# Kernel optimization log

Hardware: AMD Instinct MI355X
Metric: run time of the kernel (lower is better)

The kernel has to match this reference:

```python
import jax, jax.numpy as jnp
import numpy as np

N, D, H, F = 4096, 512, 8, 2048
DH = D // H
EPS = 1e-5


def layer_norm(x, g, b):
    mu = jnp.mean(x, axis=-1, keepdims=True)
    var = jnp.var(x, axis=-1, keepdims=True)
    return (x - mu) * jax.lax.rsqrt(var + EPS) * g + b


def setup_inputs() -> dict:
    key = jax.random.key(0)
    ks = jax.random.split(key, 16)
    s = 0.02
    return {
        "x": jax.random.normal(ks[0], (N, D), jnp.float32),
        "attention_bias": jax.random.normal(ks[1], (N, N, H), jnp.float32),
        "ln1_g": jnp.ones((D,), jnp.float32),
        "ln1_b": jnp.zeros((D,), jnp.float32),
        "wq": jax.random.normal(ks[2], (D, D), jnp.float32) * s,
        "bq": jnp.zeros((D,), jnp.float32),
        "wk": jax.random.normal(ks[3], (D, D), jnp.float32) * s,
        "bk": jnp.zeros((D,), jnp.float32),
        "wv": jax.random.normal(ks[4], (D, D), jnp.float32) * s,
        "bv": jnp.zeros((D,), jnp.float32),
        "wo": jax.random.normal(ks[5], (D, D), jnp.float32) * s,
        "bo": jnp.zeros((D,), jnp.float32),
        "ln2_g": jnp.ones((D,), jnp.float32),
        "ln2_b": jnp.zeros((D,), jnp.float32),
        "w1": jax.random.normal(ks[6], (D, F), jnp.float32) * s,
        "b1": jnp.zeros((F,), jnp.float32),
        "w2": jax.random.normal(ks[7], (F, D), jnp.float32) * s,
        "b2": jnp.zeros((D,), jnp.float32),
    }


def reference(x, attention_bias, ln1_g, ln1_b, wq, bq, wk, bk, wv, bv, wo, bo,
              ln2_g, ln2_b, w1, b1, w2, b2):
    # --- Pre-LN attention block ---
    residual = x
    xn = layer_norm(x, ln1_g, ln1_b)
    q = (xn @ wq + bq).reshape(N, H, DH)
    k = (xn @ wk + bk).reshape(N, H, DH)
    v = (xn @ wv + bv).reshape(N, H, DH)
    # scores: (H, N, N)
    scores = jnp.einsum("nhd,mhd->hnm", q, k) / jnp.sqrt(jnp.float32(DH))
    scores = scores + jnp.transpose(attention_bias, (2, 0, 1))
    attn = jax.nn.softmax(scores, axis=-1)
    ctx = jnp.einsum("hnm,mhd->nhd", attn, v).reshape(N, D)
    x = residual + (ctx @ wo + bo)
    # --- Pre-LN FFN block ---
    residual = x
    xn = layer_norm(x, ln2_g, ln2_b)
    h = jax.nn.gelu(xn @ w1 + b1, approximate=False)
    x = residual + (h @ w2 + b2)
    return x
```

## Files before the change

kernel.cpp:

```cpp
#include <hip/hip_runtime.h>


typedef float f32x4 __attribute__((ext_vector_type(4)));
typedef short s8v  __attribute__((ext_vector_type(8)));
typedef unsigned short u16;

#define MFMA16(a,b,c) __builtin_amdgcn_mfma_f32_16x16x32_bf16((a),(b),(c),0,0,0)

static constexpr int N  = 4096;
static constexpr int D  = 512;
static constexpr int H  = 8;
static constexpr int F  = 2048;
static constexpr int QKVW = 3 * D;
static constexpr int NH   = N * H;
static constexpr int QT   = 64;
static constexpr int MS   = 4;
static constexpr int ATTN_LDS = 131072;

__device__ inline u16 f2bf(float f) {
  union { float f; unsigned u; } x; x.f = f;
  unsigned r = x.u + 0x7fffu + ((x.u >> 16) & 1u);
  return (u16)(r >> 16);
}
__device__ inline float bf2f(u16 u) {
  union { unsigned u; float f; } x; x.u = ((unsigned)u) << 16;
  return x.f;
}

typedef const unsigned __attribute__((address_space(1)))* gp_t;
typedef unsigned __attribute__((address_space(3)))* lp_t;
__device__ inline void gl_lds16(const void* g, void* l) {
  __builtin_amdgcn_global_load_lds((gp_t)g, (lp_t)l, 16, 0, 0);
}

__global__ __launch_bounds__(256) void ln_kernel(const float* __restrict__ x,
                                                 const float* __restrict__ g,
                                                 const float* __restrict__ b,
                                                 u16* __restrict__ out) {
  const int row  = blockIdx.x * 4 + (threadIdx.x >> 6);
  const int lane = threadIdx.x & 63;
  const float4* xr = (const float4*)(x + (size_t)row * D);
  float4 v0 = xr[lane], v1 = xr[64 + lane];
  float s  = v0.x + v0.y + v0.z + v0.w + v1.x + v1.y + v1.z + v1.w;
  float ss = v0.x*v0.x + v0.y*v0.y + v0.z*v0.z + v0.w*v0.w
           + v1.x*v1.x + v1.y*v1.y + v1.z*v1.z + v1.w*v1.w;
  for (int off = 1; off < 64; off <<= 1) {
    s  += __shfl_xor(s,  off);
    ss += __shfl_xor(ss, off);
  }
  const float mu   = s * (1.0f / D);
  const float var  = ss * (1.0f / D) - mu * mu;
  const float rstd = rsqrtf(var + 1e-5f);
  const float4* g4 = (const float4*)g;
  const float4* b4 = (const float4*)b;
  float4 g0 = g4[lane], g1 = g4[64 + lane];
  float4 b0 = b4[lane], b1 = b4[64 + lane];
  u16* orow = out + (size_t)row * D;
  ushort4 o0, o1;
  o0.x = f2bf((v0.x - mu) * rstd * g0.x + b0.x);
  o0.y = f2bf((v0.y - mu) * rstd * g0.y + b0.y);
  o0.z = f2bf((v0.z - mu) * rstd * g0.z + b0.z);
  o0.w = f2bf((v0.w - mu) * rstd * g0.w + b0.w);
  o1.x = f2bf((v1.x - mu) * rstd * g1.x + b1.x);
  o1.y = f2bf((v1.y - mu) * rstd * g1.y + b1.y);
  o1.z = f2bf((v1.z - mu) * rstd * g1.z + b1.z);
  o1.w = f2bf((v1.w - mu) * rstd * g1.w + b1.w);
  ((ushort4*)orow)[lane]      = o0;
  ((ushort4*)orow)[64 + lane] = o1;
}

__global__ __launch_bounds__(256) void transpose_all(
    const float* __restrict__ wq, const float* __restrict__ wk,
    const float* __restrict__ wv, const float* __restrict__ wo,
    const float* __restrict__ w1, const float* __restrict__ w2,
    u16* __restrict__ WqkvT, u16* __restrict__ WoT,
    u16* __restrict__ W1T, u16* __restrict__ W2T) {
  __shared__ u16 tl[32][33];
  const int b = blockIdx.x;
  const float* src; u16* dst; int R, C, tb;
  if (b < 768)       { int m = b >> 8; tb = b & 255;
                       src = (m == 0) ? wq : (m == 1) ? wk : wv;
                       dst = WqkvT + m * D * D; R = D; C = D; }
  else if (b < 1024) { tb = b - 768;  src = wo; dst = WoT; R = D; C = D; }
  else if (b < 2048) { tb = b - 1024; src = w1; dst = W1T; R = D; C = F; }
  else               { tb = b - 2048; src = w2; dst = W2T; R = F; C = D; }
  const int tx = C / 32;
  const int cb = tb % tx, rb = tb / tx;
  const int c = threadIdx.x & 31, r8 = threadIdx.x >> 5;
#pragma unroll
  for (int i = 0; i < 4; i++) {
    int r = r8 + i * 8;
    tl[r][c] = f2bf(src[(size_t)(rb * 32 + r) * C + cb * 32 + c]);
  }
  __syncthreads();
#pragma unroll
  for (int i = 0; i < 4; i++) {
    int r = r8 + i * 8;
    dst[(size_t)(cb * 32 + r) * R + rb * 32 + c] = tl[c][r];
  }
}

__global__ void pack_bqkv(const float* __restrict__ bq, const float* __restrict__ bk,
                          const float* __restrict__ bv, float* __restrict__ bqkv) {
  int i = blockIdx.x * 256 + threadIdx.x;
  if (i < QKVW) bqkv[i] = (i < D) ? bq[i] : (i < 2 * D) ? bk[i - D] : bv[i - 2 * D];
}

__global__ void make_kvtiles(const u16* __restrict__ qkv,
                             u16* __restrict__ kt, u16* __restrict__ vt) {
  if (blockIdx.x < 1024) {
    int t = blockIdx.x * 256 + threadIdx.x;
    int ln = t & 63, half = (t >> 6) & 1, h = (t >> 7) & 7, mt = t >> 10;
    int lr = ln & 15, lq = ln >> 4;
    const u16* src = qkv + (size_t)(mt * 16 + lr) * QKVW + D + h * 64 + half * 32 + lq * 8;
    *(int4*)(kt + (size_t)t * 8) = *(const int4*)src;
  } else {
    int t = (blockIdx.x - 1024) * 256 + threadIdx.x;
    int ln = t & 63, db = (t >> 6) & 3, h = (t >> 8) & 7, mt32 = t >> 11;
    int lr = ln & 15, lq = ln >> 4;
    s8v v;
#pragma unroll
    for (int e = 0; e < 8; e++) {
      int msrc = 4 * lq + 16 * (e >> 2) + (e & 3);
      v[e] = (short)qkv[(size_t)(mt32 * 32 + msrc) * QKVW + 2 * D + h * 64 + db * 16 + lr];
    }
    *(s8v*)(vt + (size_t)t * 8) = v;
  }
}

template <int MODE>
__global__ __launch_bounds__(256) void gemm_bt(const u16* __restrict__ A,
                                               const u16* __restrict__ Bt,
                                               const float* __restrict__ bias,
                                               const float* __restrict__ res,
                                               void* __restrict__ outv,
                                               int M, int Nn, int K) {
  __shared__ __align__(16) u16 As[128 * 32];
  __shared__ __align__(16) u16 Bs[128 * 32];
  const int t = threadIdx.x;
  const int lane = t & 63, w = t >> 6;
  const int wr = w >> 1, wc = w & 1;
  const int lr = lane & 15, lq = lane >> 4;
  const int r0 = blockIdx.y * 128, c0 = blockIdx.x * 128;
  const int srow = lane >> 2, scc = (lane & 3) * 8;
  f32x4 acc[4][4] = {};
  for (int k0 = 0; k0 < K; k0 += 32) {
    __syncthreads();
#pragma unroll
    for (int s = w; s < 8; s += 4) {
      gl_lds16(&A[(size_t)(r0 + s * 16 + srow) * K + k0 + scc], &As[s * 512]);
      gl_lds16(&Bt[(size_t)(c0 + s * 16 + srow) * K + k0 + scc], &Bs[s * 512]);
    }
    __syncthreads();
    s8v af[4], bf[4];
#pragma unroll
    for (int m = 0; m < 4; m++) af[m] = *(const s8v*)&As[(wr * 64 + m * 16 + lr) * 32 + lq * 8];
#pragma unroll
    for (int n = 0; n < 4; n++) bf[n] = *(const s8v*)&Bs[(wc * 64 + n * 16 + lr) * 32 + lq * 8];
#pragma unroll
    for (int m = 0; m < 4; m++)
#pragma unroll
      for (int n = 0; n < 4; n++) acc[m][n] = MFMA16(af[m], bf[n], acc[m][n]);
  }
#pragma unroll
  for (int m = 0; m < 4; m++)
#pragma unroll
    for (int n = 0; n < 4; n++) {
      const int col = c0 + wc * 64 + n * 16 + lr;
      const float bcol = bias[col];
#pragma unroll
      for (int j = 0; j < 4; j++) {
        const int row = r0 + wr * 64 + m * 16 + lq * 4 + j;
        float v = acc[m][n][j] + bcol;
        if (MODE == 0) {
          ((u16*)outv)[(size_t)row * Nn + col] = f2bf(v);
        } else if (MODE == 1) {
          v = 0.5f * v * (1.0f + erff(v * 0.70710678118654752f));
          ((u16*)outv)[(size_t)row * Nn + col] = f2bf(v);
        } else {
          ((float*)outv)[(size_t)row * Nn + col] = v + res[(size_t)row * Nn + col];
        }
      }
    }
  (void)M;
}

__global__ __launch_bounds__(256) void gemm_bt64(const u16* __restrict__ A,
                                                 const u16* __restrict__ Bt,
                                                 const float* __restrict__ bias,
                                                 const float* __restrict__ res,
                                                 float* __restrict__ out,
                                                 int M, int Nn, int K) {
  __shared__ __align__(16) u16 As[64 * 32];
  __shared__ __align__(16) u16 Bs[128 * 32];
  const int t = threadIdx.x;
  const int lane = t & 63, w = t >> 6;
  const int wr = w >> 1, wc = w & 1;
  const int lr = lane & 15, lq = lane >> 4;
  const int r0 = blockIdx.y * 64, c0 = blockIdx.x * 128;
  const int srow = lane >> 2, scc = (lane & 3) * 8;
  f32x4 acc[2][4] = {};
  for (int k0 = 0; k0 < K; k0 += 32) {
    __syncthreads();
    gl_lds16(&A[(size_t)(r0 + w * 16 + srow) * K + k0 + scc], &As[w * 512]);
#pragma unroll
    for (int s = w; s < 8; s += 4)
      gl_lds16(&Bt[(size_t)(c0 + s * 16 + srow) * K + k0 + scc], &Bs[s * 512]);
    __syncthreads();
    s8v af[2], bf[4];
#pragma unroll
    for (int m = 0; m < 2; m++) af[m] = *(const s8v*)&As[(wr * 32 + m * 16 + lr) * 32 + lq * 8];
#pragma unroll
    for (int n = 0; n < 4; n++) bf[n] = *(const s8v*)&Bs[(wc * 64 + n * 16 + lr) * 32 + lq * 8];
#pragma unroll
    for (int m = 0; m < 2; m++)
#pragma unroll
      for (int n = 0; n < 4; n++) acc[m][n] = MFMA16(af[m], bf[n], acc[m][n]);
  }
#pragma unroll
  for (int m = 0; m < 2; m++)
#pragma unroll
    for (int n = 0; n < 4; n++) {
      const int col = c0 + wc * 64 + n * 16 + lr;
      const float bcol = bias[col];
#pragma unroll
      for (int j = 0; j < 4; j++) {
        const int row = r0 + wr * 32 + m * 16 + lq * 4 + j;
        out[(size_t)row * Nn + col] = acc[m][n][j] + bcol + res[(size_t)row * Nn + col];
      }
    }
  (void)M;
}

__global__ __launch_bounds__(512, 2) void attn_kernel(const u16* __restrict__ qkv,
                                                      const u16* __restrict__ kt,
                                                      const u16* __restrict__ vt,
                                                      const float* __restrict__ bias,
                                                      u16* __restrict__ ctxp,
                                                      float* __restrict__ ml) {
  extern __shared__ __align__(16) char smem[];
  const int tid = threadIdx.x, lane = tid & 63, h = tid >> 6;
  const int lr = lane & 15, lq = lane >> 4;
  const int bid = blockIdx.x;
  const int ms = (bid & 7) >> 1;
  const int qb = ((bid >> 3) << 1) | (bid & 1);
  const int q0 = qb * QT;
  const int mt32_0 = ms * 32;

  float4 breg[8];
  auto load_bias = [&](int t) {
#pragma unroll
    for (int i = 0; i < 8; i++) {
      int g = i * 512 + tid;
      int q = g >> 6, cc = g & 63;
      breg[i] = *(const float4*)(bias + (size_t)(q0 + q) * NH
                + (size_t)((mt32_0 + t) * 32 + (cc >> 1)) * H + (cc & 1) * 4);
    }
  };
  auto write_bias = [&](int buf) {
    float* bl = (float*)(smem + buf * 65536);
#pragma unroll
    for (int i = 0; i < 8; i++) {
      int g = i * 512 + tid;
      int q = g >> 6, cc = g & 63;
      int m = cc >> 1, h0 = (cc & 1) * 4;
      int mp = m ^ ((q & 7) << 2);
#pragma unroll
      for (int e = 0; e < 4; e++)
        bl[q * 256 + (h0 + e) * 32 + mp] = breg[i][e];
    }
  };

  s8v qf[4][2];
#pragma unroll
  for (int qc = 0; qc < 4; qc++) {
    const u16* qp = qkv + (size_t)(q0 + qc * 16 + lr) * QKVW + h * 64 + lq * 8;
    qf[qc][0] = *(const s8v*)qp;
    qf[qc][1] = *(const s8v*)(qp + 32);
  }

  f32x4 cacc[4][4] = {};
  float mrun[4], lsum[4];
#pragma unroll
  for (int qc = 0; qc < 4; qc++) { mrun[qc] = -1e30f; lsum[qc] = 0.0f; }

  load_bias(0);
  write_bias(0);
  __syncthreads();

  for (int t = 0; t < 32; t++) {
    const int mt = (mt32_0 + t) * 2;
    s8v kf[4];
    {
      const u16* kp0 = kt + ((size_t)(mt * 8 + h) * 2) * 512 + lane * 8;
      const u16* kp1 = kt + ((size_t)((mt + 1) * 8 + h) * 2) * 512 + lane * 8;
      kf[0] = *(const s8v*)kp0;
      kf[1] = *(const s8v*)(kp0 + 512);
      kf[2] = *(const s8v*)kp1;
      kf[3] = *(const s8v*)(kp1 + 512);
    }
    s8v vf[4];
    {
      const u16* vp = vt + ((size_t)((mt32_0 + t) * 8 + h) * 4) * 512 + lane * 8;
#pragma unroll
      for (int db = 0; db < 4; db++) vf[db] = *(const s8v*)(vp + (size_t)db * 512);
    }
    if (t + 1 < 32) load_bias(t + 1);

    const float* bl = (const float*)(smem + (t & 1) * 65536);
#pragma unroll
    for (int qc = 0; qc < 4; qc++) {
      f32x4 s0 = {}, s1 = {};
      s0 = MFMA16(kf[0], qf[qc][0], s0);
      s0 = MFMA16(kf[1], qf[qc][1], s0);
      s1 = MFMA16(kf[2], qf[qc][0], s1);
      s1 = MFMA16(kf[3], qf[qc][1], s1);
      const int q = qc * 16 + lr;
      const int sw = (q & 7) << 2;
      const float* blq = bl + q * 256 + h * 32;
      float p[8];
      float tmax = -1e30f;
#pragma unroll
      for (int s = 0; s < 2; s++) {
        f32x4 b4 = *(const f32x4*)(blq + ((s * 16 + lq * 4) ^ sw));
#pragma unroll
        for (int j = 0; j < 4; j++) {
          const float sv = (s ? s1[j] : s0[j]) * 0.125f + b4[j];
          p[s * 4 + j] = sv;
          tmax = fmaxf(tmax, sv);
        }
      }
      tmax = fmaxf(tmax, __shfl_xor(tmax, 16));
      tmax = fmaxf(tmax, __shfl_xor(tmax, 32));
      if (!__all(tmax <= mrun[qc])) {
        float mnew = fmaxf(mrun[qc], tmax);
        float sc = __expf(mrun[qc] - mnew);
        mrun[qc] = mnew;
        lsum[qc] *= sc;
#pragma unroll
        for (int db = 0; db < 4; db++) cacc[qc][db] *= sc;
      }
      float psum = 0.0f;
#pragma unroll
      for (int j = 0; j < 8; j++) { p[j] = __expf(p[j] - mrun[qc]); psum += p[j]; }
      lsum[qc] += psum;
      union { unsigned u[4]; s8v v; } pa;
      asm("v_cvt_pk_bf16_f32 %0, %1, %2" : "=v"(pa.u[0]) : "v"(p[0]), "v"(p[1]));
      asm("v_cvt_pk_bf16_f32 %0, %1, %2" : "=v"(pa.u[1]) : "v"(p[2]), "v"(p[3]));
      asm("v_cvt_pk_bf16_f32 %0, %1, %2" : "=v"(pa.u[2]) : "v"(p[4]), "v"(p[5]));
      asm("v_cvt_pk_bf16_f32 %0, %1, %2" : "=v"(pa.u[3]) : "v"(p[6]), "v"(p[7]));
#pragma unroll
      for (int db = 0; db < 4; db++) cacc[qc][db] = MFMA16(vf[db], pa.v, cacc[qc][db]);
    }
    if (t + 1 < 32) write_bias((t + 1) & 1);
    __syncthreads();
  }

#pragma unroll
  for (int qc = 0; qc < 4; qc++) {
    lsum[qc] += __shfl_xor(lsum[qc], 16);
    lsum[qc] += __shfl_xor(lsum[qc], 32);
  }
  if (lq == 0) {
#pragma unroll
    for (int qc = 0; qc < 4; qc++) {
      float2 v = make_float2(mrun[qc], lsum[qc]);
      *(float2*)(ml + (((size_t)ms * N + q0 + qc * 16 + lr) * H + h) * 2) = v;
    }
  }
#pragma unroll
  for (int qc = 0; qc < 4; qc++)
#pragma unroll
    for (int db = 0; db < 4; db++) {
      const size_t q = q0 + qc * 16 + lr;
      ushort4 r4;
      r4.x = f2bf(cacc[qc][db][0]);
      r4.y = f2bf(cacc[qc][db][1]);
      r4.z = f2bf(cacc[qc][db][2]);
      r4.w = f2bf(cacc[qc][db][3]);
      *(ushort4*)(ctxp + ((size_t)ms * N + q) * D + h * 64 + db * 16 + lq * 4) = r4;
    }
}

__global__ __launch_bounds__(256) void attn_merge(const u16* __restrict__ ctxp,
                                                  const float* __restrict__ ml,
                                                  u16* __restrict__ ctx) {
  int idx = blockIdx.x * 256 + threadIdx.x;
  int q = idx >> 7, c = idx & 127;
  int d0 = c * 4, h = c >> 4;
  float m_[MS], l_[MS], M = -1e30f;
#pragma unroll
  for (int s = 0; s < MS; s++) {
    float2 v = *(const float2*)(ml + (((size_t)s * N + q) * H + h) * 2);
    m_[s] = v.x; l_[s] = v.y;
    M = fmaxf(M, v.x);
  }
  float L = 0.0f, w_[MS];
#pragma unroll
  for (int s = 0; s < MS; s++) { w_[s] = __expf(m_[s] - M); L += l_[s] * w_[s]; }
  const float inv = 1.0f / L;
  float o0 = 0.0f, o1 = 0.0f, o2 = 0.0f, o3 = 0.0f;
#pragma unroll
  for (int s = 0; s < MS; s++) {
    ushort4 pv = *(const ushort4*)(ctxp + ((size_t)s * N + q) * D + d0);
    o0 += bf2f(pv.x) * w_[s];
    o1 += bf2f(pv.y) * w_[s];
    o2 += bf2f(pv.z) * w_[s];
    o3 += bf2f(pv.w) * w_[s];
  }
  ushort4 r;
  r.x = f2bf(o0 * inv); r.y = f2bf(o1 * inv);
  r.z = f2bf(o2 * inv); r.w = f2bf(o3 * inv);
  *(ushort4*)(ctx + (size_t)q * D + d0) = r;
}

extern "C" void kernel_launch(void* const* d_in, const int* in_sizes, int n_in,
                              void* d_out, int out_size, void* d_ws, size_t ws_size,
                              hipStream_t stream) {
  const float* x    = (const float*)d_in[0];
  const float* abias= (const float*)d_in[1];
  const float* ln1g = (const float*)d_in[2];
  const float* ln1b = (const float*)d_in[3];
  const float* wq   = (const float*)d_in[4];
  const float* bq   = (const float*)d_in[5];
  const float* wk   = (const float*)d_in[6];
  const float* bk   = (const float*)d_in[7];
  const float* wv   = (const float*)d_in[8];
  const float* bv   = (const float*)d_in[9];
  const float* wo   = (const float*)d_in[10];
  const float* bo   = (const float*)d_in[11];
  const float* ln2g = (const float*)d_in[12];
  const float* ln2b = (const float*)d_in[13];
  const float* w1   = (const float*)d_in[14];
  const float* b1   = (const float*)d_in[15];
  const float* w2   = (const float*)d_in[16];
  const float* b2   = (const float*)d_in[17];
  float* out = (float*)d_out;

  char* ws = (char*)d_ws;
  size_t off = 0;
  auto alloc = [&](size_t bytes) { size_t o = off; off = (off + bytes + 255) & ~(size_t)255; return (void*)(ws + o); };
  u16*   xn    = (u16*)alloc((size_t)N * D * 2);
  u16*   qkv   = (u16*)alloc((size_t)N * QKVW * 2);
  u16*   ktl   = (u16*)alloc((size_t)N * D * 2);
  u16*   vtl   = (u16*)alloc((size_t)N * D * 2);
  u16*   ctx   = (u16*)alloc((size_t)N * D * 2);
  float* x2    = (float*)alloc((size_t)N * D * 4);
  u16*   xn2   = (u16*)alloc((size_t)N * D * 2);
  u16*   hb    = (u16*)alloc((size_t)N * F * 2);
  u16*   WqkvT = (u16*)alloc((size_t)QKVW * D * 2);
  u16*   WoT   = (u16*)alloc((size_t)D * D * 2);
  u16*   W1T   = (u16*)alloc((size_t)F * D * 2);
  u16*   W2T   = (u16*)alloc((size_t)D * F * 2);
  float* bqkv  = (float*)alloc((size_t)QKVW * 4);
  u16*   ctxp  = (u16*)alloc((size_t)MS * N * D * 2);
  float* ml    = (float*)alloc((size_t)MS * N * H * 2 * 4);

  hipFuncSetAttribute((const void*)attn_kernel,
                      hipFuncAttributeMaxDynamicSharedMemorySize, ATTN_LDS);

  transpose_all<<<3072, 256, 0, stream>>>(wq, wk, wv, wo, w1, w2,
                                          WqkvT, WoT, W1T, W2T);
  pack_bqkv<<<(QKVW + 255) / 256, 256, 0, stream>>>(bq, bk, bv, bqkv);

  ln_kernel<<<N / 4, 256, 0, stream>>>(x, ln1g, ln1b, xn);
  gemm_bt<0><<<dim3(QKVW / 128, N / 128), 256, 0, stream>>>(xn, WqkvT, bqkv, nullptr, qkv, N, QKVW, D);
  make_kvtiles<<<2048, 256, 0, stream>>>(qkv, ktl, vtl);
  attn_kernel<<<(N / QT) * MS, 512, ATTN_LDS, stream>>>(qkv, ktl, vtl, abias, ctxp, ml);
  attn_merge<<<(N * 128) / 256, 256, 0, stream>>>(ctxp, ml, ctx);
  gemm_bt64<<<dim3(D / 128, N / 64), 256, 0, stream>>>(ctx, WoT, bo, x, x2, N, D, D);
  ln_kernel<<<N / 4, 256, 0, stream>>>(x2, ln2g, ln2b, xn2);
  gemm_bt<1><<<dim3(F / 128, N / 128), 256, 0, stream>>>(xn2, W1T, b1, nullptr, hb, N, F, D);
  gemm_bt64<<<dim3(D / 128, N / 64), 256, 0, stream>>>(hb, W2T, b2, x2, out, N, D, F);
  (void)in_sizes; (void)n_in; (void)out_size; (void)ws_size;
}
```

Measured before the change: 269.6 us.

## Deepen attention bias prefetch to two tiles with dual register buffers

The attention kernel now keeps two register buffers for the bias tile and issues global loads two tiles ahead instead of one, manually unrolling the key loop by two. This gives the strided bias reads more time to arrive before their values are written to LDS, hiding more global-memory latency. It doubles the bias register footprint (64 extra VGPRs), which may cause spills or reduce occupancy under the 512-thread, 2-block launch bounds.

```diff
diff --git a/kernel.cpp b/kernel.cpp
--- a/kernel.cpp
+++ b/kernel.cpp
@@ -247,17 +247,17 @@
   const int q0 = qb * QT;
   const int mt32_0 = ms * 32;
 
-  float4 breg[8];
-  auto load_bias = [&](int t) {
+  float4 bregA[8], bregB[8];
+  auto load_bias = [&](float4* br, int t) {
 #pragma unroll
     for (int i = 0; i < 8; i++) {
       int g = i * 512 + tid;
       int q = g >> 6, cc = g & 63;
-      breg[i] = *(const float4*)(bias + (size_t)(q0 + q) * NH
-                + (size_t)((mt32_0 + t) * 32 + (cc >> 1)) * H + (cc & 1) * 4);
+      br[i] = *(const float4*)(bias + (size_t)(q0 + q) * NH
+              + (size_t)((mt32_0 + t) * 32 + (cc >> 1)) * H + (cc & 1) * 4);
     }
   };
-  auto write_bias = [&](int buf) {
+  auto write_bias = [&](const float4* br, int buf) {
     float* bl = (float*)(smem + buf * 65536);
 #pragma unroll
     for (int i = 0; i < 8; i++) {
@@ -267,7 +267,7 @@
       int mp = m ^ ((q & 7) << 2);
 #pragma unroll
       for (int e = 0; e < 4; e++)
-        bl[q * 256 + (h0 + e) * 32 + mp] = breg[i][e];
+        bl[q * 256 + (h0 + e) * 32 + mp] = br[i][e];
     }
   };
 
@@ -284,11 +284,7 @@
 #pragma unroll
   for (int qc = 0; qc < 4; qc++) { mrun[qc] = -1e30f; lsum[qc] = 0.0f; }
 
-  load_bias(0);
-  write_bias(0);
-  __syncthreads();
-
-  for (int t = 0; t < 32; t++) {
+  auto do_tile = [&](int t, int buf) {
     const int mt = (mt32_0 + t) * 2;
     s8v kf[4];
     {
@@ -305,9 +301,7 @@
 #pragma unroll
       for (int db = 0; db < 4; db++) vf[db] = *(const s8v*)(vp + (size_t)db * 512);
     }
-    if (t + 1 < 32) load_bias(t + 1);
-
-    const float* bl = (const float*)(smem + (t & 1) * 65536);
+    const float* bl = (const float*)(smem + buf * 65536);
 #pragma unroll
     for (int qc = 0; qc < 4; qc++) {
       f32x4 s0 = {}, s1 = {};
@@ -352,7 +346,22 @@
 #pragma unroll
       for (int db = 0; db < 4; db++) cacc[qc][db] = MFMA16(vf[db], pa.v, cacc[qc][db]);
     }
-    if (t + 1 < 32) write_bias((t + 1) & 1);
+  };
+
+  load_bias(bregA, 0);
+  load_bias(bregB, 1);
+  write_bias(bregA, 0);
+  __syncthreads();
+
+  for (int tt = 0; tt < 16; tt++) {
+    const int t0 = tt * 2, t1 = t0 + 1;
+    if (t0 + 2 < 32) load_bias(bregA, t0 + 2);
+    do_tile(t0, 0);
+    write_bias(bregB, 1);
+    __syncthreads();
+    if (t1 + 2 < 32) load_bias(bregB, t1 + 2);
+    do_tile(t1, 1);
+    if (t1 + 1 < 32) write_bias(bregA, 0);
     __syncthreads();
   }
 
```

Result: slower. 459.0 us (+70.3%).
